# Performance work log

Measured on AMD Instinct MI355X. Metric: run time of the kernel, lower is better.

## Reference

```python
import jax, jax.numpy as jnp
import numpy as np

NSIDE = 64
LMAX = 96
MMAX = 96
NLAT = 4 * NSIDE - 1
B, C = 4, 64


def healpix_nlon_ring(t, nside):
    if 0 <= t < nside - 1:
        return 4 * (t + 1)
    if t <= 3 * nside - 1:
        return 4 * nside
    return 4 * (4 * nside - t - 1)


NLON = [healpix_nlon_ring(t, NSIDE) for t in range(NLAT)]


def healpix_latitude_theta(nside):
    t = np.arange(0, 4 * nside - 1).astype(np.float64)
    z = np.zeros_like(t)
    m1 = t < nside - 1
    m2 = (t >= nside - 1) & (t <= 3 * nside - 1)
    m3 = (t > 3 * nside - 1) & (t <= 4 * nside - 2)
    z[m1] = 1 - (t[m1] + 1) ** 2 / (3 * nside ** 2)
    z[m2] = 4 / 3 - 2 * (t[m2] + 1) / (3 * nside)
    z[m3] = (4 * nside - 1 - t[m3]) ** 2 / (3 * nside ** 2) - 1
    return np.arccos(z)


def healpix_longitude_offset(mmax, nside):
    t = np.arange(0, 4 * nside - 1).astype(np.float64)
    shift = 0.5
    tt = np.zeros_like(t)
    tt = np.where((t + 1 >= nside) & (t + 1 <= 3 * nside), shift * ((t - nside + 2) % 2) * np.pi / (2 * nside), tt)
    tt = np.where(t + 1 > 3 * nside, shift * np.pi / (2 * (4 * nside - t - 1)), tt)
    tt = np.where(t + 1 < nside, shift * np.pi / (2 * (t + 1)), tt)
    return np.einsum('t,m->tm', tt, np.arange(0, mmax).astype(np.float64))


def legpoly(mmax, lmax, x, norm='ortho', inverse=False, csphase=True):
    # (-1)^m c^l_m P^l_m(x), shape (mmax, lmax, len(x)); faithful numpy copy
    nmax = max(mmax, lmax)
    vdm = np.zeros((nmax, nmax, len(x)), dtype=np.float64)
    norm_factor = 1.0 if norm == 'ortho' else np.sqrt(4 * np.pi)
    norm_factor = 1.0 / norm_factor if inverse else norm_factor
    vdm[0, 0, :] = norm_factor / np.sqrt(4 * np.pi)
    for n in range(1, nmax):
        vdm[n - 1, n, :] = np.sqrt(2 * n + 1) * x * vdm[n - 1, n - 1, :]
        vdm[n, n, :] = np.sqrt((2 * n + 1) * (1 + x) * (1 - x) / 2 / n) * vdm[n - 1, n - 1, :]
    for n in range(2, nmax):
        for m in range(0, n - 1):
            vdm[m, n, :] = (x * np.sqrt((2 * n - 1) / (n - m) * (2 * n + 1) / (n + m)) * vdm[m, n - 1, :]
                            - np.sqrt((n + m - 1) / (n - m) * (2 * n + 1) / (2 * n - 3) * (n - m - 1) / (n + m)) * vdm[m, n - 2, :])
    if norm == 'schmidt':
        for num in range(0, nmax):
            if inverse:
                vdm[:, num, :] = vdm[:, num, :] * np.sqrt(2 * num + 1)
            else:
                vdm[:, num, :] = vdm[:, num, :] / np.sqrt(2 * num + 1)
    vdm = vdm[:mmax, :lmax]
    if csphase:
        vdm[1::2] *= -1
    return vdm


def setup_inputs() -> dict:
    key = jax.random.key(0)
    k1, k2 = jax.random.split(key)
    x_real = jax.random.normal(k1, (B, C, LMAX, MMAX), dtype=jnp.float32)
    x_imag = jax.random.normal(k2, (B, C, LMAX, MMAX), dtype=jnp.float32)
    theta = healpix_latitude_theta(NSIDE)
    pct = legpoly(MMAX, LMAX, np.cos(theta), norm='ortho', inverse=True, csphase=True)  # (M, L, NLAT)
    offset = healpix_longitude_offset(MMAX, NSIDE)  # (NLAT, M)
    return {
        'x_real': x_real,
        'x_imag': x_imag,
        'pct': jnp.asarray(pct, dtype=jnp.float32),
        'offset': jnp.asarray(offset, dtype=jnp.float32),
    }


def reference(x_real, x_imag, pct, offset):
    # Legendre transform: (..., l, m) x (m, l, k) -> (..., k=nlat, m)
    rl = jnp.einsum('...lm,mlk->...km', x_real, pct)
    im = jnp.einsum('...lm,mlk->...km', x_imag, pct)
    x = (rl + 1j * im) * jnp.exp(1j * offset)  # (..., NLAT, MMAX) complex64
    # ragged per-ring irfft: group rings sharing the same nlon into one batched irfft
    groups = {}
    for t, n in enumerate(NLON):
        groups.setdefault(n, []).append(t)
    ring_out = [None] * NLAT
    for n, idxs in groups.items():
        y = jnp.fft.irfft(x[..., jnp.asarray(idxs), :], n=n, axis=-1, norm='forward')  # (..., g, n)
        for i, t in enumerate(idxs):
            ring_out[t] = y[..., i, :]
    return jnp.concatenate(ring_out, axis=-1)  # (..., 12*nside^2)
```

## Files before the change

kernel.cpp:

```cpp
#include <hip/hip_runtime.h>
#include <hip/hip_bf16.h>
#include <math.h>

#define NLAT 255
#define NPIX 49152
#define PI_F 3.14159265358979323846f

typedef _Float16 half_t;
typedef half_t half8 __attribute__((ext_vector_type(8)));
typedef half_t half2_t __attribute__((ext_vector_type(2)));
typedef float  f32x4 __attribute__((ext_vector_type(4)));

__device__ __forceinline__ void ring_params(int t, int& n, int& roff) {
    if (t < 63)        { n = 4 * (t + 1); roff = 2 * t * (t + 1); }
    else if (t <= 191) { n = 256;         roff = 8064 + 256 * (t - 63); }
    else               { int w = 255 - t; n = 4 * w; roff = 49152 - 2 * w * (w + 1); }
}

__device__ __forceinline__ float ring_alpha(int t) {
    return (t < 63)   ? PI_F / (4.0f * (float)(t + 1))
         : (t <= 191) ? ((((t - 62) & 1)) ? PI_F / 256.0f : 0.0f)
         :              PI_F / (4.0f * (float)(255 - t));
}

__global__ __launch_bounds__(256) void k_prep(
        const float* __restrict__ pct,
        const float* __restrict__ xr, const float* __restrict__ xi,
        half_t* __restrict__ pctT, half_t* __restrict__ xh) {
    __shared__ float smem[96 * 33];
    const int bx  = blockIdx.x;
    const int tid = threadIdx.x;

    if (bx < 768) {
        const int m = bx >> 3, t0 = (bx & 7) * 32;
        for (int idx = tid; idx < 96 * 32; idx += 256) {
            int l = idx >> 5, tt = idx & 31, t = t0 + tt;
            smem[l * 33 + tt] = (t < NLAT) ? pct[((size_t)m * 96 + l) * NLAT + t] : 0.f;
        }
        __syncthreads();
        for (int idx = tid; idx < 96 * 32; idx += 256) {
            int tt = idx / 96, l = idx - tt * 96;
            pctT[((size_t)m * 256 + t0 + tt) * 96 + l] = (half_t)smem[l * 33 + tt];
        }
    } else {
        const int id  = bx - 768;
        const int z   = id / 768;
        const int rem = id - z * 768;
        const int l   = rem % 96;
        const int bc0 = (rem / 96) * 32;
        const int comp = z / 3, m0 = (z % 3) * 32;
        const float* in = comp ? xi : xr;
        const int tx = tid & 31, ty = tid >> 5;
#pragma unroll
        for (int j = 0; j < 4; ++j) {
            int bcl = ty + j * 8;
            smem[bcl * 33 + tx] = in[((size_t)(bc0 + bcl) * 96 + l) * 96 + m0 + tx];
        }
        __syncthreads();
#pragma unroll
        for (int j = 0; j < 4; ++j) {
            int ml = ty + j * 8;
            xh[((((size_t)(comp * 96 + m0 + ml)) * 12 + (l >> 3)) * 256 + bc0 + tx) * 8
               + (l & 7)] = (half_t)smem[tx * 33 + ml];
        }
    }
}

__global__ __launch_bounds__(256) void k_leg(
        const half_t* __restrict__ pctT, const half_t* __restrict__ xh,
        half_t* __restrict__ Xp) {
    const int b   = blockIdx.x;
    const int wg  = (b & 7) * 96 + (b >> 3);
    const int mg  = wg >> 5;
    const int rem = wg & 31;
    const int t0  = (rem >> 3) * 64;
    const int bc0 = (rem & 7) * 32;
    const int wid = threadIdx.x >> 6, lane = threadIdx.x & 63;
    const int wm = wid & 1, wn = wid >> 1;
    const int row = lane & 15, quad = lane >> 4;
    const int tbase = t0 + wm * 32;
    const int bc    = bc0 + wn * 16 + row;

    f32x4 acc[4][2][2];
#pragma unroll
    for (int a = 0; a < 4; ++a)
#pragma unroll
        for (int bb = 0; bb < 2; ++bb)
#pragma unroll
            for (int d = 0; d < 2; ++d) acc[a][bb][d] = (f32x4)0.f;

#pragma unroll
    for (int k0 = 0; k0 < 96; k0 += 32) {
        const int kA = k0 + quad * 8;
        half8 af[4][2], bf[4][2];
#pragma unroll
        for (int mi = 0; mi < 4; ++mi) {
            const int m = mg * 4 + mi;
#pragma unroll
            for (int mt = 0; mt < 2; ++mt)
                af[mi][mt] = *(const half8*)(pctT +
                    ((size_t)m * 256 + tbase + mt * 16 + row) * 96 + kA);
#pragma unroll
            for (int c = 0; c < 2; ++c)
                bf[mi][c] = *(const half8*)(xh +
                    ((((size_t)(c * 96 + m)) * 12 + (k0 >> 3) + quad) * 256 + bc) * 8);
        }
#pragma unroll
        for (int mi = 0; mi < 4; ++mi)
#pragma unroll
            for (int c = 0; c < 2; ++c)
#pragma unroll
                for (int mt = 0; mt < 2; ++mt)
                    acc[mi][c][mt] = __builtin_amdgcn_mfma_f32_16x16x32_f16(
                        af[mi][mt], bf[mi][c], acc[mi][c][mt], 0, 0, 0);
    }

#pragma unroll
    for (int mt = 0; mt < 2; ++mt)
#pragma unroll
        for (int r = 0; r < 4; ++r) {
            const int t = tbase + mt * 16 + quad * 4 + r;
            half8 v;
#pragma unroll
            for (int mi = 0; mi < 4; ++mi) {
                v[2 * mi]     = (half_t)acc[mi][0][mt][r];
                v[2 * mi + 1] = (half_t)acc[mi][1][mt][r];
            }
            *(half8*)(Xp + (((size_t)t * 24 + mg) * 256 + bc) * 8) = v;
        }
}

__global__ __launch_bounds__(256) void k_dft(
        const half_t* __restrict__ Xp, float* __restrict__ out) {
    __shared__ half_t Alds[6 * 4 * 64 * 8];
    const int bid = blockIdx.x;
    const int xcd = bid & 7, sub = bid >> 3;
    const int wg  = (xcd < 4 ? xcd * 128 : 512 + (xcd - 4) * 127) + sub;
    const int t   = wg >> 2;
    const int p0  = (wg & 3) * 64;
    int n, roff; ring_params(t, n, roff);
    if (p0 >= n) return;

    const int tid = threadIdx.x;
    const int wid = tid >> 6, lane = tid & 63;
    const int row = lane & 15, quad = lane >> 4;

    const int n2 = n >> 1;
    const int mh = min(95, n2);
    const int ks = (2 * (mh + 1) + 31) >> 5;

    {
        const float alpha = ring_alpha(t);
        const float invn  = 1.0f / (float)n;
        const int npairs = ks << 10;
        for (int idx = tid; idx < npairs; idx += 256) {
            const int mloc = idx & 15;
            const int prow = (idx >> 4) & 63;
            const int kk   = idx >> 10;
            const int m    = kk * 16 + mloc;
            const float phi = 6.28318530717958647692f * (float)(p0 + prow) * invn
                            + alpha;
            const float sc = (m == 0) ? 1.f : (m < n2) ? 2.f : (m == n2) ? 1.f : 0.f;
            float s, c;
            __sincosf((float)m * phi, &s, &c);
            half2_t v; v[0] = (half_t)(sc * c); v[1] = (half_t)(-sc * s);
            const int pos = (((kk * 4 + (prow >> 4)) * 64
                             + (mloc >> 2) * 16 + (prow & 15)) * 8
                             + (mloc & 3) * 2);
            *(half2_t*)(Alds + pos) = v;
        }
    }
    __syncthreads();

    const half_t* xpb = Xp + (((size_t)t * 24 + quad) * 256 + wid * 64 + row) * 8;
    const half_t* alb = Alds + (size_t)lane * 8;

    f32x4 acc[4][4];
#pragma unroll
    for (int i = 0; i < 4; ++i)
#pragma unroll
        for (int j = 0; j < 4; ++j) acc[i][j] = (f32x4)0.f;

    auto step = [&](int kk) {
        half8 b[4], a[4];
#pragma unroll
        for (int bn = 0; bn < 4; ++bn)
            b[bn] = *(const half8*)(xpb + kk * 8192 + bn * 128);
#pragma unroll
        for (int pi = 0; pi < 4; ++pi)
            a[pi] = *(const half8*)(alb + (kk * 4 + pi) * 512);
#pragma unroll
        for (int pi = 0; pi < 4; ++pi)
#pragma unroll
            for (int bn = 0; bn < 4; ++bn)
                acc[pi][bn] = __builtin_amdgcn_mfma_f32_16x16x32_f16(
                    a[pi], b[bn], acc[pi][bn], 0, 0, 0);
    };

    if (ks == 6) {
#pragma unroll
        for (int kk = 0; kk < 6; ++kk) step(kk);
    } else {
        for (int kk = 0; kk < ks; ++kk) step(kk);
    }

#pragma unroll
    for (int pi = 0; pi < 4; ++pi) {
        const int p = p0 + pi * 16 + quad * 4;
        if (p < n) {
#pragma unroll
            for (int bn = 0; bn < 4; ++bn) {
                const int bc = wid * 64 + bn * 16 + row;
                float4 v = make_float4(acc[pi][bn][0], acc[pi][bn][1],
                                       acc[pi][bn][2], acc[pi][bn][3]);
                *(float4*)(out + (size_t)bc * NPIX + roff + p) = v;
            }
        }
    }
}

extern "C" void kernel_launch(void* const* d_in, const int* in_sizes, int n_in,
                              void* d_out, int out_size, void* d_ws, size_t ws_size,
                              hipStream_t stream) {
    const float* xr  = (const float*)d_in[0];
    const float* xi  = (const float*)d_in[1];
    const float* pct = (const float*)d_in[2];
    float* out = (float*)d_out;

    char* ws = (char*)d_ws;
    half_t* pctT = (half_t*)ws;
    half_t* xh   = (half_t*)(ws + 4718592);
    half_t* Xp   = (half_t*)(ws + 4718592 + 9437184);

    k_prep<<<dim3(5376), 256, 0, stream>>>(pct, xr, xi, pctT, xh);
    k_leg <<<dim3(768), 256, 0, stream>>>(pctT, xh, Xp);
    k_dft <<<dim3(1020), 256, 0, stream>>>(Xp, out);
}
```

Measured before the change: 133.8 us.

## Vectorize x transpose in prep kernel and prefetch DFT B-fragments before twiddle build

The x-conversion part of the prep kernel now has each block handle 8 l-values at once. It reads the input with float4 loads and writes full half8 vectors, so there are fewer, wider global transactions and fewer blocks (576 instead of 4608). The DFT kernel issues the first two k-steps of Xp global loads before computing the twiddle table in LDS, so that load latency overlaps the sincos work. The cost is higher LDS use per prep block and extra registers held in the DFT kernel.

```diff
diff --git a/kernel.cpp b/kernel.cpp
--- a/kernel.cpp
+++ b/kernel.cpp
@@ -27,7 +27,7 @@
         const float* __restrict__ pct,
         const float* __restrict__ xr, const float* __restrict__ xi,
         half_t* __restrict__ pctT, half_t* __restrict__ xh) {
-    __shared__ float smem[96 * 33];
+    __shared__ float smem[8 * 32 * 33];
     const int bx  = blockIdx.x;
     const int tid = threadIdx.x;
 
@@ -43,25 +43,36 @@
             pctT[((size_t)m * 256 + t0 + tt) * 96 + l] = (half_t)smem[l * 33 + tt];
         }
     } else {
-        const int id  = bx - 768;
-        const int z   = id / 768;
-        const int rem = id - z * 768;
-        const int l   = rem % 96;
-        const int bc0 = (rem / 96) * 32;
+        const int id   = bx - 768;
+        const int lc   = id % 12;
+        const int bc0  = ((id / 12) & 7) * 32;
+        const int z    = id / 96;
         const int comp = z / 3, m0 = (z % 3) * 32;
         const float* in = comp ? xi : xr;
-        const int tx = tid & 31, ty = tid >> 5;
+
+#pragma unroll
+        for (int it = 0; it < 8; ++it) {
+            int idx = tid + it * 256;
+            int m4  = idx & 7;
+            int b   = (idx >> 3) & 31;
+            int li  = idx >> 8;
+            float4 v = *(const float4*)(in
+                + (size_t)(bc0 + b) * 9216 + (lc * 8 + li) * 96 + m0 + m4 * 4);
+            float* s = &smem[li * 1056 + b * 33 + m4 * 4];
+            s[0] = v.x; s[1] = v.y; s[2] = v.z; s[3] = v.w;
+        }
+        __syncthreads();
+
 #pragma unroll
         for (int j = 0; j < 4; ++j) {
-            int bcl = ty + j * 8;
-            smem[bcl * 33 + tx] = in[((size_t)(bc0 + bcl) * 96 + l) * 96 + m0 + tx];
-        }
-        __syncthreads();
-#pragma unroll
-        for (int j = 0; j < 4; ++j) {
-            int ml = ty + j * 8;
-            xh[((((size_t)(comp * 96 + m0 + ml)) * 12 + (l >> 3)) * 256 + bc0 + tx) * 8
-               + (l & 7)] = (half_t)smem[tx * 33 + ml];
+            int ml = (tid >> 5) + j * 8;
+            int bc = tid & 31;
+            half8 v;
+#pragma unroll
+            for (int li = 0; li < 8; ++li)
+                v[li] = (half_t)smem[li * 1056 + bc * 33 + ml];
+            *(half8*)(xh + ((((size_t)(comp * 96 + m0 + ml)) * 12 + lc) * 256
+                            + bc0 + bc) * 8) = v;
         }
     }
 }
@@ -148,6 +159,15 @@
     const int n2 = n >> 1;
     const int mh = min(95, n2);
     const int ks = (2 * (mh + 1) + 31) >> 5;
+
+    const half_t* xpb = Xp + (((size_t)t * 24 + quad) * 256 + wid * 64 + row) * 8;
+
+    half8 bpre[2][4];
+#pragma unroll
+    for (int kk = 0; kk < 2; ++kk)
+#pragma unroll
+        for (int bn = 0; bn < 4; ++bn)
+            bpre[kk][bn] = *(const half8*)(xpb + kk * 8192 + bn * 128);
 
     {
         const float alpha = ring_alpha(t);
@@ -172,7 +192,6 @@
     }
     __syncthreads();
 
-    const half_t* xpb = Xp + (((size_t)t * 24 + quad) * 256 + wid * 64 + row) * 8;
     const half_t* alb = Alds + (size_t)lane * 8;
 
     f32x4 acc[4][4];
@@ -181,11 +200,8 @@
 #pragma unroll
         for (int j = 0; j < 4; ++j) acc[i][j] = (f32x4)0.f;
 
-    auto step = [&](int kk) {
-        half8 b[4], a[4];
-#pragma unroll
-        for (int bn = 0; bn < 4; ++bn)
-            b[bn] = *(const half8*)(xpb + kk * 8192 + bn * 128);
+    auto step = [&](int kk, const half8 b[4]) {
+        half8 a[4];
 #pragma unroll
         for (int pi = 0; pi < 4; ++pi)
             a[pi] = *(const half8*)(alb + (kk * 4 + pi) * 512);
@@ -196,12 +212,25 @@
                 acc[pi][bn] = __builtin_amdgcn_mfma_f32_16x16x32_f16(
                     a[pi], b[bn], acc[pi][bn], 0, 0, 0);
     };
+    auto ldb = [&](int kk, half8 b[4]) {
+#pragma unroll
+        for (int bn = 0; bn < 4; ++bn)
+            b[bn] = *(const half8*)(xpb + kk * 8192 + bn * 128);
+    };
 
     if (ks == 6) {
-#pragma unroll
-        for (int kk = 0; kk < 6; ++kk) step(kk);
+        step(0, bpre[0]);
+        step(1, bpre[1]);
+#pragma unroll
+        for (int kk = 2; kk < 6; ++kk) {
+            half8 b[4]; ldb(kk, b); step(kk, b);
+        }
     } else {
-        for (int kk = 0; kk < ks; ++kk) step(kk);
+        step(0, bpre[0]);
+        if (ks > 1) step(1, bpre[1]);
+        for (int kk = 2; kk < ks; ++kk) {
+            half8 b[4]; ldb(kk, b); step(kk, b);
+        }
     }
 
 #pragma unroll
@@ -232,7 +261,7 @@
     half_t* xh   = (half_t*)(ws + 4718592);
     half_t* Xp   = (half_t*)(ws + 4718592 + 9437184);
 
-    k_prep<<<dim3(5376), 256, 0, stream>>>(pct, xr, xi, pctT, xh);
+    k_prep<<<dim3(768 + 576), 256, 0, stream>>>(pct, xr, xi, pctT, xh);
     k_leg <<<dim3(768), 256, 0, stream>>>(pctT, xh, Xp);
     k_dft <<<dim3(1020), 256, 0, stream>>>(Xp, out);
 }
```

New measurement: 123.1 us. -8.0%, faster.
